# Kernel tuning notes

Hardware: AMD Instinct MI355X
Metric: run time of the kernel (lower is better)

The kernel has to match this reference:

```python
import jax, jax.numpy as jnp
import numpy as np

EPS = 1e-5

def conv1d_same(x, w, b):
    # x: [B,C,T], w: [O,I,K], b: [O]
    y = jax.lax.conv_general_dilated(x, w, window_strides=(1,), padding='SAME',
                                     dimension_numbers=('NCH', 'OIH', 'NCH'))
    return y + b[None, :, None]

def bn_eval(x, gamma, beta):
    # running_mean=0, running_var=1 (fresh BatchNorm1d in eval mode)
    inv = 1.0 / jnp.sqrt(1.0 + EPS)
    return x * (gamma * inv)[None, :, None] + beta[None, :, None]

def gelu(x):
    return jax.nn.gelu(x, approximate=False)

def conv_block(x, c1w, c1b, c2w, c2b, g1, be1, g2, be2, skw=None, skb=None):
    res = x if skw is None else jnp.einsum('bct,oc->bot', x, skw[:, :, 0]) + skb[None, :, None]
    h = gelu(bn_eval(conv1d_same(x, c1w, c1b), g1, be1))
    h = bn_eval(conv1d_same(h, c2w, c2b), g2, be2)
    return gelu(h + res)

def setup_inputs() -> dict:
    key = jax.random.key(0)
    ks = jax.random.split(key, 32)
    B, C, T = 1024, 271, 281
    H, H2, E, NCLS, NSUBJ = 128, 256, 16, 1854, 4
    g = lambda i, shape, s=0.02: jax.random.normal(ks[i], shape, dtype=jnp.float32) * s
    inp = {}
    inp['X'] = jax.random.normal(ks[0], (B, C, T), dtype=jnp.float32)
    inp['subject_idxs'] = jax.random.randint(ks[1], (B,), 0, NSUBJ, dtype=jnp.int32)
    inp['attention'] = jax.random.normal(ks[2], (C, C), dtype=jnp.float32)
    inp['sa_w'] = g(3, (H, C), 0.05)
    inp['sa_b'] = jnp.zeros((H,), jnp.float32)
    inp['subj_w'] = g(4, (NSUBJ, H, H), 0.05)
    inp['subj_b'] = jnp.zeros((NSUBJ, H), jnp.float32)
    # block1: 128->128 (identity skip)
    inp['b1_c1w'] = g(5, (H, H, 3)); inp['b1_c1b'] = jnp.zeros((H,), jnp.float32)
    inp['b1_c2w'] = g(6, (H, H, 3)); inp['b1_c2b'] = jnp.zeros((H,), jnp.float32)
    inp['b1_g1'] = jnp.ones((H,), jnp.float32); inp['b1_be1'] = jnp.zeros((H,), jnp.float32)
    inp['b1_g2'] = jnp.ones((H,), jnp.float32); inp['b1_be2'] = jnp.zeros((H,), jnp.float32)
    # block2: 128->256 (1x1 conv skip)
    inp['b2_c1w'] = g(7, (H2, H, 3)); inp['b2_c1b'] = jnp.zeros((H2,), jnp.float32)
    inp['b2_c2w'] = g(8, (H2, H2, 3)); inp['b2_c2b'] = jnp.zeros((H2,), jnp.float32)
    inp['b2_g1'] = jnp.ones((H2,), jnp.float32); inp['b2_be1'] = jnp.zeros((H2,), jnp.float32)
    inp['b2_g2'] = jnp.ones((H2,), jnp.float32); inp['b2_be2'] = jnp.zeros((H2,), jnp.float32)
    inp['b2_skw'] = g(9, (H2, H, 1)); inp['b2_skb'] = jnp.zeros((H2,), jnp.float32)
    # block3: 256->256 (identity skip)
    inp['b3_c1w'] = g(10, (H2, H2, 3)); inp['b3_c1b'] = jnp.zeros((H2,), jnp.float32)
    inp['b3_c2w'] = g(11, (H2, H2, 3)); inp['b3_c2b'] = jnp.zeros((H2,), jnp.float32)
    inp['b3_g1'] = jnp.ones((H2,), jnp.float32); inp['b3_be1'] = jnp.zeros((H2,), jnp.float32)
    inp['b3_g2'] = jnp.ones((H2,), jnp.float32); inp['b3_be2'] = jnp.zeros((H2,), jnp.float32)
    # subject embedding + head
    inp['emb'] = g(12, (NSUBJ, E), 1.0)
    inp['head_w1'] = g(13, (H, H2 + E), 0.05); inp['head_b1'] = jnp.zeros((H,), jnp.float32)
    inp['head_w2'] = g(14, (NCLS, H), 0.05); inp['head_b2'] = jnp.zeros((NCLS,), jnp.float32)
    return inp

def reference(X, subject_idxs, attention, sa_w, sa_b, subj_w, subj_b,
              b1_c1w, b1_c1b, b1_c2w, b1_c2b, b1_g1, b1_be1, b1_g2, b1_be2,
              b2_c1w, b2_c1b, b2_c2w, b2_c2b, b2_g1, b2_be1, b2_g2, b2_be2, b2_skw, b2_skb,
              b3_c1w, b3_c1b, b3_c2w, b3_c2b, b3_g1, b3_be1, b3_g2, b3_be2,
              emb, head_w1, head_b1, head_w2, head_b2):
    # SpatialAttention
    attn = jax.nn.softmax(attention, axis=1)            # [C,C]
    x = jnp.einsum('bct,ic->bit', X, attn)              # [B,C,T]
    x = jnp.einsum('bit,oi->bot', x, sa_w) + sa_b[None, :, None]  # [B,H,T]
    # Per-subject 1x1 conv: batched gather of weights instead of python loop
    Ws = subj_w[subject_idxs]                           # [B,H,H]
    bs = subj_b[subject_idxs]                           # [B,H]
    x = jnp.einsum('bct,boc->bot', x, Ws) + bs[:, :, None]
    # ConvBlock stack
    x = conv_block(x, b1_c1w, b1_c1b, b1_c2w, b1_c2b, b1_g1, b1_be1, b1_g2, b1_be2)
    x = conv_block(x, b2_c1w, b2_c1b, b2_c2w, b2_c2b, b2_g1, b2_be1, b2_g2, b2_be2, b2_skw, b2_skb)
    x = conv_block(x, b3_c1w, b3_c1b, b3_c2w, b3_c2b, b3_g1, b3_be1, b3_g2, b3_be2)
    # Head: global avg pool over time, concat subject embedding, MLP
    x = jnp.mean(x, axis=2)                             # [B,2H]
    x = jnp.concatenate([x, emb[subject_idxs]], axis=1) # [B,2H+E]
    h = jax.nn.relu(x @ head_w1.T + head_b1)
    return h @ head_w2.T + head_b2                      # [B,num_classes]
```

## Files before the change

kernel.cpp:

```cpp
#include <hip/hip_runtime.h>
#include <hip/hip_bf16.h>
#include <math.h>

constexpr int Bz = 1024;
constexpr int C0 = 271;
constexpr int CP0 = 288;
constexpr int Tt = 281;
constexpr int H1 = 128;
constexpr int H2 = 256;
constexpr int NCLS = 1854;
constexpr int ED = 16;
constexpr float BN_INV = 0.9999950000374996f;

typedef __attribute__((ext_vector_type(8))) short s16x8;
typedef __attribute__((ext_vector_type(16))) float f32x16;

__device__ __forceinline__ float gelu_f(float v) {
    return 0.5f * v * (1.0f + erff(v * 0.7071067811865475f));
}
__device__ __forceinline__ float bf2f(short s) {
    return __builtin_bit_cast(float, ((unsigned int)(unsigned short)s) << 16);
}
__device__ __forceinline__ short f2bf(float f) {
    return __builtin_bit_cast(short, __float2bfloat16(f));
}


__global__ void softmax_rows_k(const float* __restrict__ a, float* __restrict__ o, int n) {
    __shared__ float red[256];
    const int row = blockIdx.x, tid = threadIdx.x;
    const float* r = a + (size_t)row * n;
    float m = -1e30f;
    for (int i = tid; i < n; i += 256) m = fmaxf(m, r[i]);
    red[tid] = m; __syncthreads();
    for (int s = 128; s > 0; s >>= 1) { if (tid < s) red[tid] = fmaxf(red[tid], red[tid + s]); __syncthreads(); }
    m = red[0]; __syncthreads();
    float acc = 0.f;
    for (int i = tid; i < n; i += 256) acc += expf(r[i] - m);
    red[tid] = acc; __syncthreads();
    for (int s = 128; s > 0; s >>= 1) { if (tid < s) red[tid] += red[tid + s]; __syncthreads(); }
    const float inv = 1.0f / red[0];
    for (int i = tid; i < n; i += 256) o[(size_t)row * n + i] = expf(r[i] - m) * inv;
}

__global__ void gemm_M_k(const float* __restrict__ sa_w, const float* __restrict__ attnS,
                         float* __restrict__ M) {
    int idx = blockIdx.x * 256 + threadIdx.x;
    if (idx >= H1 * C0) return;
    int o = idx / C0, c = idx - o * C0;
    float s = 0.f;
    for (int i = 0; i < C0; ++i) s = fmaf(sa_w[(size_t)o * C0 + i], attnS[(size_t)i * C0 + c], s);
    M[idx] = s;
}

__global__ void msubA_k(const float* __restrict__ subj_w, const float* __restrict__ M,
                        short* __restrict__ wA) {
    int idx = blockIdx.x * 256 + threadIdx.x;
    if (idx >= 4 * 9 * 128 * 32) return;
    int j = idx & 31;
    int r = idx >> 5;
    int o = r & 127;
    int r2 = r >> 7;
    int cc = r2 % 9;
    int s = r2 / 9;
    int c = cc * 32 + j;
    float a = 0.f;
    if (c < C0) {
        const float* wr = subj_w + ((size_t)s * 128 + o) * 128;
        for (int h = 0; h < 128; ++h) a = fmaf(wr[h], M[(size_t)h * C0 + c], a);
    }
    wA[idx] = f2bf(a);
}

__global__ void biasS_k(const float* __restrict__ subj_w, const float* __restrict__ sa_b,
                        const float* __restrict__ subj_b, float* __restrict__ biasS) {
    int idx = blockIdx.x * 256 + threadIdx.x;
    if (idx >= 4 * H1) return;
    int s = idx >> 7, o = idx & 127;
    const float* wr = subj_w + ((size_t)s * H1 + o) * H1;
    float a = subj_b[idx];
    for (int h = 0; h < H1; ++h) a = fmaf(wr[h], sa_b[h], a);
    biasS[idx] = a;
}

__global__ void wprep_k(const float* __restrict__ w, short* __restrict__ o_,
                        int CIN, int O, int K, int NC) {
    int idx = blockIdx.x * 256 + threadIdx.x;
    int total = NC * K * O * 32;
    if (idx >= total) return;
    int j = idx & 31;
    int r = idx >> 5;
    int o = r % O;
    int r2 = r / O;
    int k = r2 % K;
    int cc = r2 / K;
    int c = cc * 32 + j;
    float v = (c < CIN) ? w[((size_t)o * CIN + c) * K + k] : 0.f;
    o_[idx] = f2bf(v);
}

__global__ void xpose_k(const float* __restrict__ X, short* __restrict__ xT) {
    __shared__ float tile[32][33];
    int b = blockIdx.z;
    int t0 = blockIdx.x * 32, c0 = blockIdx.y * 32;
    int tx = threadIdx.x, ty = threadIdx.y;
    #pragma unroll
    for (int i = 0; i < 4; ++i) {
        int c = c0 + ty + i * 8, t = t0 + tx;
        float v = 0.f;
        if (c < C0 && t < Tt) v = X[((size_t)b * C0 + c) * Tt + t];
        tile[ty + i * 8][tx] = v;
    }
    __syncthreads();
    #pragma unroll
    for (int i = 0; i < 4; ++i) {
        int t = t0 + ty + i * 8, c = c0 + tx;
        if (t < Tt && c < CP0) xT[((size_t)b * Tt + t) * CP0 + c] = f2bf(tile[tx][ty + i * 8]);
    }
}


template<int K, int O_BLK, int NWAVE, bool GELU, bool HASRES>
__global__ __launch_bounds__(NWAVE * 64, 2)
void convCL_k(const short* __restrict__ xT, int XC, int NC,
              const short* __restrict__ wPre,
              const float* __restrict__ bias,
              const float* __restrict__ gamma, const float* __restrict__ beta,
              const short* __restrict__ res,
              short* __restrict__ out,
              const int* __restrict__ sidx, int wstride, int bstride)
{
    constexpr int NT    = NWAVE * 64;
    constexpr int PAD   = (K - 1) / 2;
    constexpr int XT    = 96 + K - 1;
    constexpr int WROWS = K * O_BLK;
    constexpr int WSH   = WROWS * 40;
    constexpr int OUTSH = 96 * O_BLK;
    constexpr int SH1   = WSH > OUTSH ? WSH : OUTSH;
    constexpr int XCHUNK = XT * 4;
    constexpr int WCHUNK = WROWS * 4;
    constexpr int O2 = O_BLK * 2;

    __shared__ __align__(16) short sh1[SH1];
    __shared__ __align__(16) short xs[XT * 40];

    const int t0  = blockIdx.x * 96;
    const int b   = blockIdx.y;
    const int tid = threadIdx.x;
    const int lane = tid & 63, wv = tid >> 6;
    const int l31 = lane & 31, hi = lane >> 5;
    const int owave = wv * 64;

    const short* wb = wPre;
    const float* bb = bias;
    if (sidx) { int s = sidx[b]; wb += (size_t)s * wstride; bb += (size_t)s * bstride; }

    f32x16 acc[2][3];
    #pragma unroll
    for (int i = 0; i < 2; ++i)
        #pragma unroll
        for (int j = 0; j < 3; ++j)
            #pragma unroll
            for (int e = 0; e < 16; ++e) acc[i][j][e] = 0.f;

    const size_t xbase = (size_t)b * Tt * XC;

    for (int cc = 0; cc < NC; ++cc) {
        __syncthreads();
        const short* wsrc = wb + (size_t)cc * (WROWS * 32);
        #pragma unroll
        for (int it = 0; it < (WCHUNK + NT - 1) / NT; ++it) {
            int q = it * NT + tid;
            if ((WCHUNK % NT) == 0 || q < WCHUNK) {
                int r = q >> 2, p = q & 3;
                *(int4*)((char*)sh1 + r * 80 + p * 16) = *(const int4*)(wsrc + (size_t)q * 8);
            }
        }
        const int cbase = cc * 32;
        #pragma unroll
        for (int it = 0; it < (XCHUNK + NT - 1) / NT; ++it) {
            int q = it * NT + tid;
            if (q < XCHUNK) {
                int r = q >> 2, p = q & 3;
                int gt = t0 + r - PAD;
                int4 v = make_int4(0, 0, 0, 0);
                if ((unsigned)gt < (unsigned)Tt)
                    v = *(const int4*)(xT + xbase + (size_t)gt * XC + cbase + p * 8);
                *(int4*)((char*)xs + r * 80 + p * 16) = v;
            }
        }
        __syncthreads();
        #pragma unroll
        for (int k = 0; k < K; ++k) {
            #pragma unroll
            for (int kk = 0; kk < 2; ++kk) {
                s16x8 af[2];
                #pragma unroll
                for (int os = 0; os < 2; ++os)
                    af[os] = *(const s16x8*)((const char*)sh1 +
                              (k * O_BLK + owave + os * 32 + l31) * 80 + kk * 32 + hi * 16);
                #pragma unroll
                for (int ts = 0; ts < 3; ++ts) {
                    s16x8 bfv = *(const s16x8*)((const char*)xs +
                                (ts * 32 + l31 + k) * 80 + kk * 32 + hi * 16);
                    #pragma unroll
                    for (int os = 0; os < 2; ++os)
                        acc[os][ts] = __builtin_amdgcn_mfma_f32_32x32x16_bf16(
                            af[os], bfv, acc[os][ts], 0, 0, 0);
                }
            }
        }
    }

    __syncthreads();
    #pragma unroll
    for (int os = 0; os < 2; ++os) {
        #pragma unroll
        for (int rq = 0; rq < 4; ++rq) {
            #pragma unroll
            for (int rp = 0; rp < 2; ++rp) {
                const int oc = owave + os * 32 + 8 * rq + rp * 2 + 4 * hi;
                const float b0 = bb[oc];
                const float b1 = bb[oc + 1];
                const float g0 = gamma ? gamma[oc] * BN_INV : 1.f;
                const float g1 = gamma ? gamma[oc + 1] * BN_INV : 1.f;
                const float e0 = beta ? beta[oc] : 0.f;
                const float e1 = beta ? beta[oc + 1] : 0.f;
                const int r0 = rq * 4 + rp * 2;
                #pragma unroll
                for (int ts = 0; ts < 3; ++ts) {
                    float v0 = (acc[os][ts][r0] + b0) * g0 + e0;
                    float v1 = (acc[os][ts][r0 + 1] + b1) * g1 + e1;
                    int tloc = ts * 32 + l31;
                    int byte = tloc * O2 + ((oc * 2) ^ ((tloc & 15) << 4));
                    __hip_bfloat162 pk;
                    pk.x = __float2bfloat16(v0);
                    pk.y = __float2bfloat16(v1);
                    *(__hip_bfloat162*)((char*)sh1 + byte) = pk;
                }
            }
        }
    }
    __syncthreads();

    constexpr int RCH = O_BLK / 8;
    const size_t obase = (size_t)b * Tt * O_BLK;
    for (int q = tid; q < 96 * RCH; q += NT) {
        int r = q / RCH, cp = q % RCH;
        int gt = t0 + r;
        if (gt >= Tt) continue;
        s16x8 hv = *(const s16x8*)((const char*)sh1 + r * O2 + ((cp * 16) ^ ((r & 15) << 4)));
        s16x8 rv;
        if (HASRES) rv = *(const s16x8*)(res + obase + (size_t)gt * O_BLK + cp * 8);
        s16x8 ov;
        #pragma unroll
        for (int j = 0; j < 8; ++j) {
            float v = bf2f(hv[j]);
            if (HASRES) v += bf2f(rv[j]);
            if (GELU) v = gelu_f(v);
            ov[j] = f2bf(v);
        }
        *(s16x8*)(out + obase + (size_t)gt * O_BLK + cp * 8) = ov;
    }
}


__global__ void poolCL_k(const short* __restrict__ x, float* __restrict__ pooled) {
    const int b = blockIdx.x;
    const int o = threadIdx.x;
    const short* p = x + (size_t)b * Tt * H2 + o;
    float s = 0.f;
    for (int t = 0; t < Tt; ++t) s += bf2f(p[(size_t)t * H2]);
    pooled[(size_t)b * H2 + o] = s * (1.0f / Tt);
}

__global__ void head1_k(const float* __restrict__ pooled, const float* __restrict__ emb,
                        const int* __restrict__ sidx, const float* __restrict__ w1,
                        const float* __restrict__ b1, float* __restrict__ hout) {
    int idx = blockIdx.x * 256 + threadIdx.x;
    if (idx >= Bz * H1) return;
    int b = idx >> 7, j = idx & 127;
    const float* wr = w1 + (size_t)j * (H2 + ED);
    const float* pr = pooled + (size_t)b * H2;
    float a = b1[j];
    for (int i = 0; i < H2; ++i) a = fmaf(pr[i], wr[i], a);
    const float* er = emb + (size_t)sidx[b] * ED;
    #pragma unroll
    for (int e = 0; e < ED; ++e) a = fmaf(er[e], wr[H2 + e], a);
    hout[idx] = fmaxf(a, 0.f);
}

__global__ __launch_bounds__(256)
void head2_k(const float* __restrict__ h, const float* __restrict__ w2,
             const float* __restrict__ b2, float* __restrict__ out) {
    const int n0 = blockIdx.x * 64;
    const int b0 = blockIdx.y * 16;
    __shared__ float hs[16][128];
    __shared__ float w2s[64][129];
    const int tid = threadIdx.x;
    for (int idx = tid; idx < 16 * 128; idx += 256) {
        int bl = idx >> 7, j = idx & 127;
        hs[bl][j] = h[(size_t)(b0 + bl) * H1 + j];
    }
    for (int idx = tid; idx < 64 * 128; idx += 256) {
        int nl = idx >> 7, j = idx & 127;
        int n = n0 + nl;
        w2s[nl][j] = (n < NCLS) ? w2[(size_t)n * H1 + j] : 0.f;
    }
    __syncthreads();
    const int nl = tid & 63, bg = tid >> 6;
    float acc[4] = {0.f, 0.f, 0.f, 0.f};
    for (int j = 0; j < 128; ++j) {
        const float wv = w2s[nl][j];
        #pragma unroll
        for (int bb = 0; bb < 4; ++bb) acc[bb] = fmaf(wv, hs[bg * 4 + bb][j], acc[bb]);
    }
    const int n = n0 + nl;
    if (n < NCLS) {
        const float bv = b2[n];
        #pragma unroll
        for (int bb = 0; bb < 4; ++bb)
            out[(size_t)(b0 + bg * 4 + bb) * NCLS + n] = acc[bb] + bv;
    }
}


extern "C" void kernel_launch(void* const* d_in, const int* in_sizes, int n_in,
                              void* d_out, int out_size, void* d_ws, size_t ws_size,
                              hipStream_t stream) {
    const float* X      = (const float*)d_in[0];
    const int*   sidx   = (const int*)  d_in[1];
    const float* attn   = (const float*)d_in[2];
    const float* sa_w   = (const float*)d_in[3];
    const float* sa_b   = (const float*)d_in[4];
    const float* subj_w = (const float*)d_in[5];
    const float* subj_b = (const float*)d_in[6];
    const float* b1c1w = (const float*)d_in[7];  const float* b1c1b = (const float*)d_in[8];
    const float* b1c2w = (const float*)d_in[9];  const float* b1c2b = (const float*)d_in[10];
    const float* b1g1  = (const float*)d_in[11]; const float* b1be1 = (const float*)d_in[12];
    const float* b1g2  = (const float*)d_in[13]; const float* b1be2 = (const float*)d_in[14];
    const float* b2c1w = (const float*)d_in[15]; const float* b2c1b = (const float*)d_in[16];
    const float* b2c2w = (const float*)d_in[17]; const float* b2c2b = (const float*)d_in[18];
    const float* b2g1  = (const float*)d_in[19]; const float* b2be1 = (const float*)d_in[20];
    const float* b2g2  = (const float*)d_in[21]; const float* b2be2 = (const float*)d_in[22];
    const float* b2skw = (const float*)d_in[23]; const float* b2skb = (const float*)d_in[24];
    const float* b3c1w = (const float*)d_in[25]; const float* b3c1b = (const float*)d_in[26];
    const float* b3c2w = (const float*)d_in[27]; const float* b3c2b = (const float*)d_in[28];
    const float* b3g1  = (const float*)d_in[29]; const float* b3be1 = (const float*)d_in[30];
    const float* b3g2  = (const float*)d_in[31]; const float* b3be2 = (const float*)d_in[32];
    const float* emb   = (const float*)d_in[33];
    const float* hw1   = (const float*)d_in[34]; const float* hb1 = (const float*)d_in[35];
    const float* hw2   = (const float*)d_in[36]; const float* hb2 = (const float*)d_in[37];
    float* out = (float*)d_out;
    (void)in_sizes; (void)n_in; (void)out_size; (void)ws_size;

    char* wsp = (char*)d_ws;
    size_t off = 0;
    auto allocF = [&](size_t n) {
        float* p = (float*)(wsp + off);
        off += ((n * sizeof(float)) + 255) & ~(size_t)255;
        return p;
    };
    auto allocS = [&](size_t n) {
        short* p = (short*)(wsp + off);
        off += ((n * sizeof(short)) + 255) & ~(size_t)255;
        return p;
    };
    float* attnS   = allocF((size_t)C0 * C0);
    float* Mmat    = allocF((size_t)H1 * C0);
    float* biasS   = allocF((size_t)4 * H1);
    float* pooled  = allocF((size_t)Bz * H2);
    float* hbuf    = allocF((size_t)Bz * H1);
    short* wStageA = allocS((size_t)4 * 9 * 128 * 32);
    short* wp_b1c1 = allocS((size_t)4 * 3 * 128 * 32);
    short* wp_b1c2 = allocS((size_t)4 * 3 * 128 * 32);
    short* wp_b2c1 = allocS((size_t)4 * 3 * 256 * 32);
    short* wp_b2c2 = allocS((size_t)8 * 3 * 256 * 32);
    short* wp_b3c1 = allocS((size_t)8 * 3 * 256 * 32);
    short* wp_b3c2 = allocS((size_t)8 * 3 * 256 * 32);
    short* wp_skip = allocS((size_t)4 * 1 * 256 * 32);
    short* xT      = allocS((size_t)Bz * Tt * CP0);
    const size_t bufsz = (size_t)Bz * Tt * H2;
    short* bufA = allocS(bufsz);
    short* bufB = allocS(bufsz);
    short* bufC = allocS(bufsz);

    softmax_rows_k<<<C0, 256, 0, stream>>>(attn, attnS, C0);
    gemm_M_k<<<(H1 * C0 + 255) / 256, 256, 0, stream>>>(sa_w, attnS, Mmat);
    msubA_k<<<(4 * 9 * 128 * 32 + 255) / 256, 256, 0, stream>>>(subj_w, Mmat, wStageA);
    biasS_k<<<2, 256, 0, stream>>>(subj_w, sa_b, subj_b, biasS);
    wprep_k<<<(4 * 3 * 128 * 32 + 255) / 256, 256, 0, stream>>>(b1c1w, wp_b1c1, 128, 128, 3, 4);
    wprep_k<<<(4 * 3 * 128 * 32 + 255) / 256, 256, 0, stream>>>(b1c2w, wp_b1c2, 128, 128, 3, 4);
    wprep_k<<<(4 * 3 * 256 * 32 + 255) / 256, 256, 0, stream>>>(b2c1w, wp_b2c1, 128, 256, 3, 4);
    wprep_k<<<(8 * 3 * 256 * 32 + 255) / 256, 256, 0, stream>>>(b2c2w, wp_b2c2, 256, 256, 3, 8);
    wprep_k<<<(8 * 3 * 256 * 32 + 255) / 256, 256, 0, stream>>>(b3c1w, wp_b3c1, 256, 256, 3, 8);
    wprep_k<<<(8 * 3 * 256 * 32 + 255) / 256, 256, 0, stream>>>(b3c2w, wp_b3c2, 256, 256, 3, 8);
    wprep_k<<<(4 * 1 * 256 * 32 + 255) / 256, 256, 0, stream>>>(b2skw, wp_skip, 128, 256, 1, 4);
    xpose_k<<<dim3(9, 9, Bz), dim3(32, 8), 0, stream>>>(X, xT);

    dim3 cgrid(3, Bz);

    convCL_k<1, 128, 2, false, false><<<cgrid, 128, 0, stream>>>(
        xT, CP0, 9, wStageA, biasS, nullptr, nullptr, nullptr, bufA, sidx, 9 * 128 * 32, 128);
    convCL_k<3, 128, 2, true, false><<<cgrid, 128, 0, stream>>>(
        bufA, 128, 4, wp_b1c1, b1c1b, b1g1, b1be1, nullptr, bufB, nullptr, 0, 0);
    convCL_k<3, 128, 2, true, true><<<cgrid, 128, 0, stream>>>(
        bufB, 128, 4, wp_b1c2, b1c2b, b1g2, b1be2, bufA, bufC, nullptr, 0, 0);
    convCL_k<1, 256, 4, false, false><<<cgrid, 256, 0, stream>>>(
        bufC, 128, 4, wp_skip, b2skb, nullptr, nullptr, nullptr, bufA, nullptr, 0, 0);
    convCL_k<3, 256, 4, true, false><<<cgrid, 256, 0, stream>>>(
        bufC, 128, 4, wp_b2c1, b2c1b, b2g1, b2be1, nullptr, bufB, nullptr, 0, 0);
    convCL_k<3, 256, 4, true, true><<<cgrid, 256, 0, stream>>>(
        bufB, 256, 8, wp_b2c2, b2c2b, b2g2, b2be2, bufA, bufC, nullptr, 0, 0);
    convCL_k<3, 256, 4, true, false><<<cgrid, 256, 0, stream>>>(
        bufC, 256, 8, wp_b3c1, b3c1b, b3g1, b3be1, nullptr, bufA, nullptr, 0, 0);
    convCL_k<3, 256, 4, true, true><<<cgrid, 256, 0, stream>>>(
        bufA, 256, 8, wp_b3c2, b3c2b, b3g2, b3be2, bufC, bufB, nullptr, 0, 0);
    poolCL_k<<<Bz, 256, 0, stream>>>(bufB, pooled);
    head1_k<<<(Bz * H1 + 255) / 256, 256, 0, stream>>>(pooled, emb, sidx, hw1, hb1, hbuf);
    head2_k<<<dim3((NCLS + 63) / 64, Bz / 16), 256, 0, stream>>>(hbuf, hw2, hb2, out);
}
```

Baseline: 1.500 ms.

## Pipeline conv kernels with async global-to-LDS loads and MFMA-fragment weight layout

```diff
diff --git a/kernel.cpp b/kernel.cpp
--- a/kernel.cpp
+++ b/kernel.cpp
@@ -6,6 +6,7 @@
 constexpr int C0 = 271;
 constexpr int CP0 = 288;
 constexpr int Tt = 281;
+constexpr int TR = 292;
 constexpr int H1 = 128;
 constexpr int H2 = 256;
 constexpr int NCLS = 1854;
@@ -25,6 +26,31 @@
     return __builtin_bit_cast(short, __float2bfloat16(f));
 }
 
+typedef unsigned int u32;
+typedef const __attribute__((address_space(1))) u32 gu32;
+typedef __attribute__((address_space(3))) u32 lu32;
+
+__device__ __forceinline__ void gl16(const void* g, void* l) {
+    __builtin_amdgcn_global_load_lds((gu32*)(uintptr_t)g, (lu32*)(uintptr_t)l, 16, 0, 0);
+}
+template<int N> __device__ __forceinline__ void waitv() {
+    asm volatile("s_waitcnt vmcnt(%0)" :: "i"(N) : "memory");
+}
+__device__ __forceinline__ void hard_barrier() {
+    __builtin_amdgcn_s_barrier();
+    __builtin_amdgcn_sched_barrier(0);
+}
+
+
+__global__ void zrows_k(short* base, int C) {
+    const int b = blockIdx.x;
+    const int n = 11 * (C / 8);
+    for (int i = threadIdx.x; i < n; i += 256) {
+        int ri = i / (C / 8), c8 = i - ri * (C / 8);
+        int row = (ri == 0) ? 0 : 281 + ri;
+        *(int4*)(base + ((size_t)b * TR + row) * C + c8 * 8) = make_int4(0, 0, 0, 0);
+    }
+}
 
 __global__ void softmax_rows_k(const float* __restrict__ a, float* __restrict__ o, int n) {
     __shared__ float red[256];
@@ -53,23 +79,37 @@
     M[idx] = s;
 }
 
+__global__ void wfrag_k(const float* __restrict__ w, short* __restrict__ out,
+                        int CIN, int O, int K, int NC) {
+    int idx = blockIdx.x * 256 + threadIdx.x;
+    int OB32 = O / 32;
+    int total = NC * K * OB32 * 2 * 512;
+    if (idx >= total) return;
+    int j = idx & 7, lane = (idx >> 3) & 63, kk = (idx >> 9) & 1, r = idx >> 10;
+    int ob = r % OB32, r2 = r / OB32;
+    int k = r2 % K, cc = r2 / K;
+    int o = ob * 32 + (lane & 31);
+    int c = cc * 32 + kk * 16 + (lane >> 5) * 8 + j;
+    float v = (c < CIN) ? w[((size_t)o * CIN + c) * K + k] : 0.f;
+    out[idx] = f2bf(v);
+}
+
 __global__ void msubA_k(const float* __restrict__ subj_w, const float* __restrict__ M,
-                        short* __restrict__ wA) {
+                        short* __restrict__ out) {
     int idx = blockIdx.x * 256 + threadIdx.x;
-    if (idx >= 4 * 9 * 128 * 32) return;
-    int j = idx & 31;
-    int r = idx >> 5;
-    int o = r & 127;
-    int r2 = r >> 7;
-    int cc = r2 % 9;
-    int s = r2 / 9;
-    int c = cc * 32 + j;
+    const int per_s = 9 * 1 * 4 * 2 * 512;
+    if (idx >= 4 * per_s) return;
+    int s = idx / per_s, rem = idx % per_s;
+    int j = rem & 7, lane = (rem >> 3) & 63, kk = (rem >> 9) & 1, r = rem >> 10;
+    int ob = r % 4, cc = r / 4;
+    int o = ob * 32 + (lane & 31);
+    int c = cc * 32 + kk * 16 + (lane >> 5) * 8 + j;
     float a = 0.f;
     if (c < C0) {
         const float* wr = subj_w + ((size_t)s * 128 + o) * 128;
         for (int h = 0; h < 128; ++h) a = fmaf(wr[h], M[(size_t)h * C0 + c], a);
     }
-    wA[idx] = f2bf(a);
+    out[idx] = f2bf(a);
 }
 
 __global__ void biasS_k(const float* __restrict__ subj_w, const float* __restrict__ sa_b,
@@ -81,22 +121,6 @@
     float a = subj_b[idx];
     for (int h = 0; h < H1; ++h) a = fmaf(wr[h], sa_b[h], a);
     biasS[idx] = a;
-}
-
-__global__ void wprep_k(const float* __restrict__ w, short* __restrict__ o_,
-                        int CIN, int O, int K, int NC) {
-    int idx = blockIdx.x * 256 + threadIdx.x;
-    int total = NC * K * O * 32;
-    if (idx >= total) return;
-    int j = idx & 31;
-    int r = idx >> 5;
-    int o = r % O;
-    int r2 = r / O;
-    int k = r2 % K;
-    int cc = r2 / K;
-    int c = cc * 32 + j;
-    float v = (c < CIN) ? w[((size_t)o * CIN + c) * K + k] : 0.f;
-    o_[idx] = f2bf(v);
 }
 
 __global__ void xpose_k(const float* __restrict__ X, short* __restrict__ xT) {
@@ -115,45 +139,52 @@
     #pragma unroll
     for (int i = 0; i < 4; ++i) {
         int t = t0 + ty + i * 8, c = c0 + tx;
-        if (t < Tt && c < CP0) xT[((size_t)b * Tt + t) * CP0 + c] = f2bf(tile[tx][ty + i * 8]);
-    }
-}
-
-
-template<int K, int O_BLK, int NWAVE, bool GELU, bool HASRES>
-__global__ __launch_bounds__(NWAVE * 64, 2)
-void convCL_k(const short* __restrict__ xT, int XC, int NC,
-              const short* __restrict__ wPre,
-              const float* __restrict__ bias,
-              const float* __restrict__ gamma, const float* __restrict__ beta,
-              const short* __restrict__ res,
-              short* __restrict__ out,
-              const int* __restrict__ sidx, int wstride, int bstride)
+        if (t < Tt) xT[((size_t)b * TR + t + 1) * CP0 + c] = f2bf(tile[tx][ty + i * 8]);
+    }
+}
+
+
+template<int K, int NC, int O_BLK, int NOW, int NB, bool GELU, bool HASRES>
+__global__ __launch_bounds__(NOW * NB * 192)
+void convMF(const short* __restrict__ xin, int XC,
+            const short* __restrict__ wfrag,
+            const float* __restrict__ bias,
+            const float* __restrict__ gamma, const float* __restrict__ beta,
+            const short* __restrict__ res, short* __restrict__ out,
+            const int* __restrict__ sidx, int wsub, int bsub)
 {
-    constexpr int NT    = NWAVE * 64;
-    constexpr int PAD   = (K - 1) / 2;
-    constexpr int XT    = 96 + K - 1;
-    constexpr int WROWS = K * O_BLK;
-    constexpr int WSH   = WROWS * 40;
-    constexpr int OUTSH = 96 * O_BLK;
-    constexpr int SH1   = WSH > OUTSH ? WSH : OUTSH;
-    constexpr int XCHUNK = XT * 4;
-    constexpr int WCHUNK = WROWS * 4;
-    constexpr int O2 = O_BLK * 2;
-
-    __shared__ __align__(16) short sh1[SH1];
-    __shared__ __align__(16) short xs[XT * 40];
-
-    const int t0  = blockIdx.x * 96;
-    const int b   = blockIdx.y;
-    const int tid = threadIdx.x;
+    constexpr int NW     = NOW * NB * 3;
+    constexpr int NT     = NW * 64;
+    constexpr int OB32   = O_BLK / 32;
+    constexpr int PAD    = (K - 1) / 2;
+    constexpr int RSTART = 1 - PAD;
+    constexpr int A_I    = K * OB32 * 2;
+    constexpr int X_I    = 18;
+    constexpr int TI     = A_I + NB * X_I;
+    constexpr int Q      = TI / NW;
+    constexpr int R      = TI % NW;
+    constexpr int QH     = (R > 0) ? Q + 1 : Q;
+    constexpr int ABYTES = A_I * 1024;
+    constexpr int X_SLOT = X_I * 1024 + 256;
+    constexpr int HALF   = ABYTES + NB * X_SLOT;
+    constexpr int O2     = O_BLK * 2;
+
+    __shared__ __align__(16) char smem[2 * HALF];
+
+    const int b0   = blockIdx.x * NB;
+    const int tid  = threadIdx.x;
     const int lane = tid & 63, wv = tid >> 6;
-    const int l31 = lane & 31, hi = lane >> 5;
-    const int owave = wv * 64;
-
-    const short* wb = wPre;
-    const float* bb = bias;
-    if (sidx) { int s = sidx[b]; wb += (size_t)s * wstride; bb += (size_t)s * bstride; }
+    const int l31  = lane & 31, hi = lane >> 5;
+    const int bqw  = wv / (NOW * 3);
+    const int w2   = wv % (NOW * 3);
+    const int wvt  = w2 / NOW;
+    const int wvo  = w2 % NOW;
+    const int tg   = wvt * 96;
+    const int Sw   = Q + (wv < R ? 1 : 0);
+
+    int subj = sidx ? sidx[b0] : 0;
+    const char*  wbase = (const char*)(wfrag + (size_t)subj * wsub);
+    const float* bb    = bias + (size_t)subj * bsub;
 
     f32x16 acc[2][3];
     #pragma unroll
@@ -163,104 +194,110 @@
             #pragma unroll
             for (int e = 0; e < 16; ++e) acc[i][j][e] = 0.f;
 
-    const size_t xbase = (size_t)b * Tt * XC;
-
-    for (int cc = 0; cc < NC; ++cc) {
-        __syncthreads();
-        const short* wsrc = wb + (size_t)cc * (WROWS * 32);
-        #pragma unroll
-        for (int it = 0; it < (WCHUNK + NT - 1) / NT; ++it) {
-            int q = it * NT + tid;
-            if ((WCHUNK % NT) == 0 || q < WCHUNK) {
+    auto issue = [&](int cc, int pb) {
+        char* base = smem + pb * HALF;
+        const char* wsrc = wbase + (size_t)cc * (A_I * 1024);
+        for (int s = 0; s < Sw; ++s) {
+            int i = s * NW + wv;
+            if (i < A_I) {
+                gl16(wsrc + (size_t)i * 1024 + lane * 16, base + i * 1024);
+            } else {
+                int xi = i - A_I;
+                int bql = xi / X_I, seg = xi - bql * X_I;
+                int q = seg * 64 + lane;
                 int r = q >> 2, p = q & 3;
-                *(int4*)((char*)sh1 + r * 80 + p * 16) = *(const int4*)(wsrc + (size_t)q * 8);
+                int ps = p ^ ((r >> 1) & 3);
+                const char* g = (const char*)xin +
+                    (((size_t)(b0 + bql) * TR + (RSTART + r)) * XC + cc * 32) * 2 + ps * 16;
+                gl16(g, base + ABYTES + bql * X_SLOT + seg * 1024);
             }
         }
-        const int cbase = cc * 32;
-        #pragma unroll
-        for (int it = 0; it < (XCHUNK + NT - 1) / NT; ++it) {
-            int q = it * NT + tid;
-            if (q < XCHUNK) {
-                int r = q >> 2, p = q & 3;
-                int gt = t0 + r - PAD;
-                int4 v = make_int4(0, 0, 0, 0);
-                if ((unsigned)gt < (unsigned)Tt)
-                    v = *(const int4*)(xT + xbase + (size_t)gt * XC + cbase + p * 8);
-                *(int4*)((char*)xs + r * 80 + p * 16) = v;
-            }
+    };
+
+    issue(0, 0);
+    int cur = 0;
+    for (int cc = 0; cc < NC; ++cc) {
+        if (cc + 1 < NC) {
+            issue(cc + 1, cur ^ 1);
+            if (wv < R) waitv<QH>(); else waitv<Q>();
+        } else {
+            waitv<0>();
         }
-        __syncthreads();
+        hard_barrier();
+
+        const char* Ab = smem + cur * HALF;
+        const char* Xb = Ab + ABYTES + bqw * X_SLOT;
         #pragma unroll
         for (int k = 0; k < K; ++k) {
             #pragma unroll
             for (int kk = 0; kk < 2; ++kk) {
-                s16x8 af[2];
-                #pragma unroll
-                for (int os = 0; os < 2; ++os)
-                    af[os] = *(const s16x8*)((const char*)sh1 +
-                              (k * O_BLK + owave + os * 32 + l31) * 80 + kk * 32 + hi * 16);
+                s16x8 a0 = *(const s16x8*)(Ab + (((k * OB32 + wvo * 2 + 0) * 2 + kk) << 10) + (lane << 4));
+                s16x8 a1 = *(const s16x8*)(Ab + (((k * OB32 + wvo * 2 + 1) * 2 + kk) << 10) + (lane << 4));
                 #pragma unroll
                 for (int ts = 0; ts < 3; ++ts) {
-                    s16x8 bfv = *(const s16x8*)((const char*)xs +
-                                (ts * 32 + l31 + k) * 80 + kk * 32 + hi * 16);
-                    #pragma unroll
-                    for (int os = 0; os < 2; ++os)
-                        acc[os][ts] = __builtin_amdgcn_mfma_f32_32x32x16_bf16(
-                            af[os], bfv, acc[os][ts], 0, 0, 0);
+                    int rl = tg + ts * 32 + l31 + k;
+                    s16x8 bv = *(const s16x8*)(Xb + rl * 64 + ((((kk << 1) | hi) ^ ((rl >> 1) & 3)) << 4));
+                    acc[0][ts] = __builtin_amdgcn_mfma_f32_32x32x16_bf16(a0, bv, acc[0][ts], 0, 0, 0);
+                    acc[1][ts] = __builtin_amdgcn_mfma_f32_32x32x16_bf16(a1, bv, acc[1][ts], 0, 0, 0);
                 }
             }
         }
-    }
-
-    __syncthreads();
-    #pragma unroll
-    for (int os = 0; os < 2; ++os) {
-        #pragma unroll
-        for (int rq = 0; rq < 4; ++rq) {
+        hard_barrier();
+        cur ^= 1;
+    }
+
+    constexpr int RCH = O_BLK / 8;
+    for (int g = 0; g < 3; ++g) {
+        __syncthreads();
+        if (wvt == g) {
             #pragma unroll
-            for (int rp = 0; rp < 2; ++rp) {
-                const int oc = owave + os * 32 + 8 * rq + rp * 2 + 4 * hi;
-                const float b0 = bb[oc];
-                const float b1 = bb[oc + 1];
-                const float g0 = gamma ? gamma[oc] * BN_INV : 1.f;
-                const float g1 = gamma ? gamma[oc + 1] * BN_INV : 1.f;
-                const float e0 = beta ? beta[oc] : 0.f;
-                const float e1 = beta ? beta[oc + 1] : 0.f;
-                const int r0 = rq * 4 + rp * 2;
+            for (int os = 0; os < 2; ++os) {
                 #pragma unroll
-                for (int ts = 0; ts < 3; ++ts) {
-                    float v0 = (acc[os][ts][r0] + b0) * g0 + e0;
-                    float v1 = (acc[os][ts][r0 + 1] + b1) * g1 + e1;
-                    int tloc = ts * 32 + l31;
-                    int byte = tloc * O2 + ((oc * 2) ^ ((tloc & 15) << 4));
-                    __hip_bfloat162 pk;
-                    pk.x = __float2bfloat16(v0);
-                    pk.y = __float2bfloat16(v1);
-                    *(__hip_bfloat162*)((char*)sh1 + byte) = pk;
+                for (int rq = 0; rq < 4; ++rq) {
+                    #pragma unroll
+                    for (int rp = 0; rp < 2; ++rp) {
+                        const int oc = wvo * 64 + os * 32 + 8 * rq + rp * 2 + 4 * hi;
+                        const float bv0 = bb[oc], bv1 = bb[oc + 1];
+                        const float g0 = gamma ? gamma[oc] * BN_INV : 1.f;
+                        const float g1 = gamma ? gamma[oc + 1] * BN_INV : 1.f;
+                        const float e0 = beta ? beta[oc] : 0.f;
+                        const float e1 = beta ? beta[oc + 1] : 0.f;
+                        const int r0 = rq * 4 + rp * 2;
+                        #pragma unroll
+                        for (int ts = 0; ts < 3; ++ts) {
+                            float v0 = (acc[os][ts][r0] + bv0) * g0 + e0;
+                            float v1 = (acc[os][ts][r0 + 1] + bv1) * g1 + e1;
+                            int tl = ts * 32 + l31;
+                            int byte = (bqw * 96 + tl) * O2 + ((oc * 2) ^ ((tl & 15) << 4));
+                            __hip_bfloat162 pk;
+                            pk.x = __float2bfloat16(v0);
+                            pk.y = __float2bfloat16(v1);
+                            *(__hip_bfloat162*)(smem + byte) = pk;
+                        }
+                    }
                 }
             }
         }
-    }
-    __syncthreads();
-
-    constexpr int RCH = O_BLK / 8;
-    const size_t obase = (size_t)b * Tt * O_BLK;
-    for (int q = tid; q < 96 * RCH; q += NT) {
-        int r = q / RCH, cp = q % RCH;
-        int gt = t0 + r;
-        if (gt >= Tt) continue;
-        s16x8 hv = *(const s16x8*)((const char*)sh1 + r * O2 + ((cp * 16) ^ ((r & 15) << 4)));
-        s16x8 rv;
-        if (HASRES) rv = *(const s16x8*)(res + obase + (size_t)gt * O_BLK + cp * 8);
-        s16x8 ov;
-        #pragma unroll
-        for (int j = 0; j < 8; ++j) {
-            float v = bf2f(hv[j]);
-            if (HASRES) v += bf2f(rv[j]);
-            if (GELU) v = gelu_f(v);
-            ov[j] = f2bf(v);
+        __syncthreads();
+        for (int qq = tid; qq < NB * 96 * RCH; qq += NT) {
+            int bql = qq / (96 * RCH), rem = qq - bql * (96 * RCH);
+            int r = rem / RCH, cp = rem - r * RCH;
+            int t = g * 96 + r;
+            if (t >= Tt) continue;
+            s16x8 hv = *(const s16x8*)(smem + (bql * 96 + r) * O2 + ((cp * 16) ^ ((r & 15) << 4)));
+            size_t orow = ((size_t)(b0 + bql) * TR + t + 1) * O_BLK + cp * 8;
+            s16x8 rv;
+            if (HASRES) rv = *(const s16x8*)(res + orow);
+            s16x8 ov;
+            #pragma unroll
+            for (int j = 0; j < 8; ++j) {
+                float v = bf2f(hv[j]);
+                if (HASRES) v += bf2f(rv[j]);
+                if (GELU) v = gelu_f(v);
+                ov[j] = f2bf(v);
+            }
+            *(s16x8*)(out + orow) = ov;
         }
-        *(s16x8*)(out + obase + (size_t)gt * O_BLK + cp * 8) = ov;
     }
 }
 
@@ -268,7 +305,7 @@
 __global__ void poolCL_k(const short* __restrict__ x, float* __restrict__ pooled) {
     const int b = blockIdx.x;
     const int o = threadIdx.x;
-    const short* p = x + (size_t)b * Tt * H2 + o;
+    const short* p = x + ((size_t)b * TR + 1) * H2 + o;
     float s = 0.f;
     for (int t = 0; t < Tt; ++t) s += bf2f(p[(size_t)t * H2]);
     pooled[(size_t)b * H2 + o] = s * (1.0f / Tt);
@@ -371,52 +408,57 @@
     float* biasS   = allocF((size_t)4 * H1);
     float* pooled  = allocF((size_t)Bz * H2);
     float* hbuf    = allocF((size_t)Bz * H1);
-    short* wStageA = allocS((size_t)4 * 9 * 128 * 32);
-    short* wp_b1c1 = allocS((size_t)4 * 3 * 128 * 32);
-    short* wp_b1c2 = allocS((size_t)4 * 3 * 128 * 32);
-    short* wp_b2c1 = allocS((size_t)4 * 3 * 256 * 32);
-    short* wp_b2c2 = allocS((size_t)8 * 3 * 256 * 32);
-    short* wp_b3c1 = allocS((size_t)8 * 3 * 256 * 32);
-    short* wp_b3c2 = allocS((size_t)8 * 3 * 256 * 32);
-    short* wp_skip = allocS((size_t)4 * 1 * 256 * 32);
-    short* xT      = allocS((size_t)Bz * Tt * CP0);
-    const size_t bufsz = (size_t)Bz * Tt * H2;
-    short* bufA = allocS(bufsz);
-    short* bufB = allocS(bufsz);
-    short* bufC = allocS(bufsz);
+    short* wStageA = allocS((size_t)4 * 9 * 4 * 2 * 512);
+    short* wp_b1c1 = allocS((size_t)4 * 3 * 4 * 2 * 512);
+    short* wp_b1c2 = allocS((size_t)4 * 3 * 4 * 2 * 512);
+    short* wp_skip = allocS((size_t)4 * 1 * 8 * 2 * 512);
+    short* wp_b2c1 = allocS((size_t)4 * 3 * 8 * 2 * 512);
+    short* wp_b2c2 = allocS((size_t)8 * 3 * 8 * 2 * 512);
+    short* wp_b3c1 = allocS((size_t)8 * 3 * 8 * 2 * 512);
+    short* wp_b3c2 = allocS((size_t)8 * 3 * 8 * 2 * 512);
+    short* xT   = allocS((size_t)Bz * TR * CP0);
+    short* bufP = allocS((size_t)Bz * TR * H1);
+    short* bufQ = allocS((size_t)Bz * TR * H1);
+    short* bufR = allocS((size_t)Bz * TR * H2);
+    short* bufS = allocS((size_t)Bz * TR * H2);
+
+    zrows_k<<<Bz, 256, 0, stream>>>(xT, CP0);
+    zrows_k<<<Bz, 256, 0, stream>>>(bufP, H1);
+    zrows_k<<<Bz, 256, 0, stream>>>(bufQ, H1);
+    zrows_k<<<Bz, 256, 0, stream>>>(bufR, H2);
+    zrows_k<<<Bz, 256, 0, stream>>>(bufS, H2);
 
     softmax_rows_k<<<C0, 256, 0, stream>>>(attn, attnS, C0);
     gemm_M_k<<<(H1 * C0 + 255) / 256, 256, 0, stream>>>(sa_w, attnS, Mmat);
-    msubA_k<<<(4 * 9 * 128 * 32 + 255) / 256, 256, 0, stream>>>(subj_w, Mmat, wStageA);
+    msubA_k<<<(4 * 36864 + 255) / 256, 256, 0, stream>>>(subj_w, Mmat, wStageA);
     biasS_k<<<2, 256, 0, stream>>>(subj_w, sa_b, subj_b, biasS);
-    wprep_k<<<(4 * 3 * 128 * 32 + 255) / 256, 256, 0, stream>>>(b1c1w, wp_b1c1, 128, 128, 3, 4);
-    wprep_k<<<(4 * 3 * 128 * 32 + 255) / 256, 256, 0, stream>>>(b1c2w, wp_b1c2, 128, 128, 3, 4);
-    wprep_k<<<(4 * 3 * 256 * 32 + 255) / 256, 256, 0, stream>>>(b2c1w, wp_b2c1, 128, 256, 3, 4);
-    wprep_k<<<(8 * 3 * 256 * 32 + 255) / 256, 256, 0, stream>>>(b2c2w, wp_b2c2, 256, 256, 3, 8);
-    wprep_k<<<(8 * 3 * 256 * 32 + 255) / 256, 256, 0, stream>>>(b3c1w, wp_b3c1, 256, 256, 3, 8);
-    wprep_k<<<(8 * 3 * 256 * 32 + 255) / 256, 256, 0, stream>>>(b3c2w, wp_b3c2, 256, 256, 3, 8);
-    wprep_k<<<(4 * 1 * 256 * 32 + 255) / 256, 256, 0, stream>>>(b2skw, wp_skip, 128, 256, 1, 4);
+    wfrag_k<<<(4*3*4*2*512 + 255) / 256, 256, 0, stream>>>(b1c1w, wp_b1c1, 128, 128, 3, 4);
+    wfrag_k<<<(4*3*4*2*512 + 255) / 256, 256, 0, stream>>>(b1c2w, wp_b1c2, 128, 128, 3, 4);
+    wfrag_k<<<(4*1*8*2*512 + 255) / 256, 256, 0, stream>>>(b2skw, wp_skip, 128, 256, 1, 4);
+    wfrag_k<<<(4*3*8*2*512 + 255) / 256, 256, 0, stream>>>(b2c1w, wp_b2c1, 128, 256, 3, 4);
+    wfrag_k<<<(8*3*8*2*512 + 255) / 256, 256, 0, stream>>>(b2c2w, wp_b2c2, 256, 256, 3, 8);
+    wfrag_k<<<(8*3*8*2*512 + 255) / 256, 256, 0, stream>>>(b3c1w, wp_b3c1, 256, 256, 3, 8);
+    wfrag_k<<<(8*3*8*2*512 + 255) / 256, 256, 0, stream>>>(b3c2w, wp_b3c2, 256, 256, 3, 8);
     xpose_k<<<dim3(9, 9, Bz), dim3(32, 8), 0, stream>>>(X, xT);
 
-    dim3 cgrid(3, Bz);
-
-    convCL_k<1, 128, 2, false, false><<<cgrid, 128, 0, stream>>>(
-        xT, CP0, 9, wStageA, biasS, nullptr, nullptr, nullptr, bufA, sidx, 9 * 128 * 32, 128);
-    convCL_k<3, 128, 2, true, false><<<cgrid, 128, 0, stream>>>(
-        bufA, 128, 4, wp_b1c1, b1c1b, b1g1, b1be1, nullptr, bufB, nullptr, 0, 0);
-    convCL_k<3, 128, 2, true, true><<<cgrid, 128, 0, stream>>>(
-        bufB, 128, 4, wp_b1c2, b1c2b, b1g2, b1be2, bufA, bufC, nullptr, 0, 0);
-    convCL_k<1, 256, 4, false, false><<<cgrid, 256, 0, stream>>>(
-        bufC, 128, 4, wp_skip, b2skb, nullptr, nullptr, nullptr, bufA, nullptr, 0, 0);
-    convCL_k<3, 256, 4, true, false><<<cgrid, 256, 0, stream>>>(
-        bufC, 128, 4, wp_b2c1, b2c1b, b2g1, b2be1, nullptr, bufB, nullptr, 0, 0);
-    convCL_k<3, 256, 4, true, true><<<cgrid, 256, 0, stream>>>(
-        bufB, 256, 8, wp_b2c2, b2c2b, b2g2, b2be2, bufA, bufC, nullptr, 0, 0);
-    convCL_k<3, 256, 4, true, false><<<cgrid, 256, 0, stream>>>(
-        bufC, 256, 8, wp_b3c1, b3c1b, b3g1, b3be1, nullptr, bufA, nullptr, 0, 0);
-    convCL_k<3, 256, 4, true, true><<<cgrid, 256, 0, stream>>>(
-        bufA, 256, 8, wp_b3c2, b3c2b, b3g2, b3be2, bufC, bufB, nullptr, 0, 0);
-    poolCL_k<<<Bz, 256, 0, stream>>>(bufB, pooled);
+    convMF<1, 9, 128, 2, 1, false, false><<<Bz, 384, 0, stream>>>(
+        xT, CP0, wStageA, biasS, nullptr, nullptr, nullptr, bufP, sidx, 36864, 128);
+    convMF<3, 4, 128, 2, 2, true, false><<<Bz / 2, 768, 0, stream>>>(
+        bufP, H1, wp_b1c1, b1c1b, b1g1, b1be1, nullptr, bufQ, nullptr, 0, 0);
+    convMF<3, 4, 128, 2, 2, true, true><<<Bz / 2, 768, 0, stream>>>(
+        bufQ, H1, wp_b1c2, b1c2b, b1g2, b1be2, bufP, bufP, nullptr, 0, 0);
+    convMF<1, 4, 256, 4, 1, false, false><<<Bz, 768, 0, stream>>>(
+        bufP, H1, wp_skip, b2skb, nullptr, nullptr, nullptr, bufS, nullptr, 0, 0);
+    convMF<3, 4, 256, 4, 1, true, false><<<Bz, 768, 0, stream>>>(
+        bufP, H1, wp_b2c1, b2c1b, b2g1, b2be1, nullptr, bufR, nullptr, 0, 0);
+    convMF<3, 8, 256, 4, 1, true, true><<<Bz, 768, 0, stream>>>(
+        bufR, H2, wp_b2c2, b2c2b, b2g2, b2be2, bufS, bufS, nullptr, 0, 0);
+    convMF<3, 8, 256, 4, 1, true, false><<<Bz, 768, 0, stream>>>(
+        bufS, H2, wp_b3c1, b3c1b, b3g1, b3be1, nullptr, bufR, nullptr, 0, 0);
+    convMF<3, 8, 256, 4, 1, true, true><<<Bz, 768, 0, stream>>>(
+        bufR, H2, wp_b3c2, b3c2b, b3g2, b3be2, bufS, bufS, nullptr, 0, 0);
+
+    poolCL_k<<<Bz, 256, 0, stream>>>(bufS, pooled);
     head1_k<<<(Bz * H1 + 255) / 256, 256, 0, stream>>>(pooled, emb, sidx, hw1, hb1, hbuf);
     head2_k<<<dim3((NCLS + 63) / 64, Bz / 16), 256, 0, stream>>>(hbuf, hw2, hb2, out);
 }
```

Result: faster. 1.333 ms (-11.2%).
